# Optimization experiments

Measured on AMD Instinct MI355X. Metric: run time of the kernel, lower is better.

## Reference

```python
import jax, jax.numpy as jnp
import numpy as np

D_MODEL = 1024
N_HEAD = 16
D_HEAD = D_MODEL // N_HEAD


def setup_inputs() -> dict:
    key = jax.random.key(0)
    ks = jax.random.split(key, 5)
    x = jax.random.normal(ks[0], (4, 2048, D_MODEL), dtype=jnp.float32)
    s = 1.0 / np.sqrt(D_MODEL)
    W_qkv = jax.random.normal(ks[1], (D_MODEL, 3 * D_MODEL), dtype=jnp.float32) * s
    b_qkv = jnp.zeros((3 * D_MODEL,), dtype=jnp.float32)
    W_out = jax.random.normal(ks[2], (D_MODEL, D_MODEL), dtype=jnp.float32) * s
    b_out = jnp.zeros((D_MODEL,), dtype=jnp.float32)
    return {"x": x, "W_qkv": W_qkv, "b_qkv": b_qkv, "W_out": W_out, "b_out": b_out}


def reference(x, W_qkv, b_qkv, W_out, b_out):
    B, T, C = x.shape
    qkv = x @ W_qkv + b_qkv                      # [B,T,3C]
    q, k, v = jnp.split(qkv, 3, axis=-1)
    def heads(t):
        return t.reshape(B, T, N_HEAD, D_HEAD).transpose(0, 2, 1, 3)  # [B,H,T,Dh]
    q, k, v = heads(q), heads(k), heads(v)
    scale = 1.0 / np.sqrt(D_HEAD)
    attn = jnp.einsum('bhqd,bhkd->bhqk', q, k) * scale  # [B,H,T,T]
    causal = jnp.tril(jnp.ones((T, T), dtype=bool))
    attn = jnp.where(causal, attn, -jnp.inf)
    attn = jax.nn.softmax(attn, axis=-1)
    out = jnp.einsum('bhqk,bhkd->bhqd', attn, v)  # [B,H,T,Dh]
    out = out.transpose(0, 2, 1, 3).reshape(B, T, C)
    return out @ W_out + b_out
```

## Files before the change

kernel.cpp:

```cpp
#include <hip/hip_runtime.h>

typedef __bf16 bf16;
typedef __bf16 bf16x4 __attribute__((ext_vector_type(4)));
typedef __bf16 bf16x8 __attribute__((ext_vector_type(8)));
typedef float f32x4 __attribute__((ext_vector_type(4)));

#define T_SEQ 2048
#define QK_LD 2048

extern "C" __device__ float __ocml_native_exp2_f32(float);

#define GLOAD16(gp, lp)                                                        \
  __builtin_amdgcn_global_load_lds(                                            \
      (const __attribute__((address_space(1))) unsigned int*)(gp),             \
      (__attribute__((address_space(3))) unsigned int*)(lp), 16, 0, 0)

__global__ void prep_kernel(const float* __restrict__ x, bf16* __restrict__ xb,
                            const float* __restrict__ Wq, bf16* __restrict__ Wtq,
                            const float* __restrict__ Wo, bf16* __restrict__ Wto) {
    __shared__ float tile[32][33];
    const int t = threadIdx.x;
    if (blockIdx.x < 8192) {
        const int i = (blockIdx.x * 256 + t) * 4;
        const float4 f = *(const float4*)(x + i);
        bf16x4 o;
        o.x = (bf16)f.x; o.y = (bf16)f.y; o.z = (bf16)f.z; o.w = (bf16)f.w;
        *(bf16x4*)(xb + i) = o;
        return;
    }
    const int bid = blockIdx.x - 8192;
    const int xblk = bid & 127, yblk = bid >> 7;
    const bool isQ = xblk < 96;
    const float* W = isQ ? Wq : Wo;
    bf16* Wt = isQ ? Wtq : Wto;
    const int C = isQ ? 3072 : 1024;
    const int R = 1024;
    const int bx = (isQ ? xblk : (xblk - 96)) * 32;
    const int by = yblk * 32;
    const int tx = t & 31, ty = t >> 5;
#pragma unroll
    for (int i = 0; i < 32; i += 8)
        tile[ty + i][tx] = W[(size_t)(by + ty + i) * C + bx + tx];
    __syncthreads();
#pragma unroll
    for (int i = 0; i < 32; i += 8)
        Wt[(size_t)(bx + ty + i) * R + by + tx] = (bf16)tile[tx][ty + i];
}

template <bool OUT_BF16, bool SPLIT_V>
__global__ __launch_bounds__(256, 2)
void gemm128(const bf16* __restrict__ A, const bf16* __restrict__ Bt,
             const float* __restrict__ bias, void* __restrict__ Cout,
             bf16* __restrict__ Vtb, int M, int N, int K, int ldC) {
    __shared__ bf16 sm[32768];

    const int t = threadIdx.x;
    const int lane = t & 63, quad = lane >> 4, l16 = lane & 15;
    const int wave = t >> 6;
    const int wm = (wave >> 1) * 64;
    const int wn = (wave & 1) * 64;
    const long m0 = (long)blockIdx.y * 128;
    const long n0 = (long)blockIdx.x * 128;
    (void)M; (void)N;

    f32x4 acc[4][4] = {};

    const int srow = t >> 3;
    const int scol = ((t & 7) ^ ((t >> 3) & 7)) * 8;
    const bf16* agp = A  + (m0 + srow) * (long)K + scol;
    const bf16* bgp = Bt + (n0 + srow) * (long)K + scol;
    const long rowK32 = (long)32 * K;

    auto stage = [&](int buf, int kt) {
        bf16* d = sm + buf * 16384 + t * 8;
        const bf16* a = agp + (long)kt * 64;
        const bf16* b = bgp + (long)kt * 64;
        GLOAD16(a,               d);
        GLOAD16(a +     rowK32,  d + 2048);
        GLOAD16(a + 2 * rowK32,  d + 4096);
        GLOAD16(a + 3 * rowK32,  d + 6144);
        GLOAD16(b,               d + 8192);
        GLOAD16(b +     rowK32,  d + 10240);
        GLOAD16(b + 2 * rowK32,  d + 12288);
        GLOAD16(b + 3 * rowK32,  d + 14336);
    };

    int offA[4][2], offB[4][2];
#pragma unroll
    for (int i = 0; i < 4; ++i)
#pragma unroll
        for (int ks = 0; ks < 2; ++ks) {
            const int rA = wm + i * 16 + l16;
            offA[i][ks] = rA * 64 + (((ks * 4 + quad) ^ (rA & 7)) << 3);
            const int rB = wn + i * 16 + l16;
            offB[i][ks] = 8192 + rB * 64 + (((ks * 4 + quad) ^ (rB & 7)) << 3);
        }

    const int nkt = K >> 6;

    stage(0, 0);
    asm volatile("s_waitcnt vmcnt(0)" ::: "memory");
    __builtin_amdgcn_s_barrier();
    __builtin_amdgcn_sched_barrier(0);

    for (int kt = 0; kt < nkt; ++kt) {
        const int buf = kt & 1;
        if (kt + 1 < nkt) stage(buf ^ 1, kt + 1);
        const bf16* base_ = sm + buf * 16384;
        bf16x8 fA[2][4], fB[2][4];
#pragma unroll
        for (int ks = 0; ks < 2; ++ks)
#pragma unroll
            for (int i = 0; i < 4; ++i) {
                fA[ks][i] = *(const bf16x8*)(base_ + offA[i][ks]);
                fB[ks][i] = *(const bf16x8*)(base_ + offB[i][ks]);
            }
#pragma unroll
        for (int ks = 0; ks < 2; ++ks)
#pragma unroll
            for (int i = 0; i < 4; ++i)
#pragma unroll
                for (int j = 0; j < 4; ++j)
                    acc[i][j] = __builtin_amdgcn_mfma_f32_16x16x32_bf16(
                        fB[ks][j], fA[ks][i], acc[i][j], 0, 0, 0);
        if (kt + 1 < nkt) {
            asm volatile("s_waitcnt vmcnt(0)" ::: "memory");
            __builtin_amdgcn_s_barrier();
            __builtin_amdgcn_sched_barrier(0);
        }
    }

    bf16*  Cb = (bf16*)Cout;
    float* Cf = (float*)Cout;
    const bool vblock = SPLIT_V && (n0 >= 2048);
#pragma unroll
    for (int i = 0; i < 4; ++i) {
        const long gm = m0 + wm + i * 16 + l16;
#pragma unroll
        for (int j = 0; j < 4; ++j) {
            const int nloc = wn + j * 16 + quad * 4;
            const long n = n0 + nloc;
            const float4 bv = *(const float4*)(bias + n);
            float v[4];
#pragma unroll
            for (int r = 0; r < 4; ++r) v[r] = acc[i][j][r] + (&bv.x)[r];
            if (vblock) {
                const int bb = (int)(gm >> 11), tok = (int)(gm & 2047);
                const int nv = (int)(n - 2048);
                const int h = nv >> 6, d0 = nv & 63;
                bf16* dst = Vtb + ((size_t)(bb * 16 + h) * 64 + d0) * T_SEQ + tok;
#pragma unroll
                for (int r = 0; r < 4; ++r) dst[(size_t)r * T_SEQ] = (bf16)v[r];
            } else if (OUT_BF16) {
                bf16x4 o;
#pragma unroll
                for (int r = 0; r < 4; ++r) o[r] = (bf16)v[r];
                *(bf16x4*)(Cb + gm * ldC + n) = o;
            } else {
                float4 o;
#pragma unroll
                for (int r = 0; r < 4; ++r) (&o.x)[r] = v[r];
                *(float4*)(Cf + gm * ldC + n) = o;
            }
        }
    }
}

__global__ __launch_bounds__(256, 3)
void attn_kernel(const bf16* __restrict__ qk, const bf16* __restrict__ vtb,
                 bf16* __restrict__ Out) {
    const int bh = blockIdx.x;
    const int qt = 15 - (int)blockIdx.y;
    const int b = bh >> 4, h = bh & 15;
    const int t = threadIdx.x;
    const int wave = t >> 6, lane = t & 63, quad = lane >> 4, l16 = lane & 15;
    const int wq = wave * 32;
    const int q0 = qt * 128;

    __shared__ bf16 Ks[2][4096];
    __shared__ bf16 VTs[2][4096];
    __shared__ bf16 Ps[8192];

    const bf16* Qg = qk + (size_t)b * T_SEQ * QK_LD + h * 64;
    const bf16* Kg = Qg + 1024;
    const bf16* vth = vtb + (size_t)bh * 64 * T_SEQ;

    for (int c = t; c < 1024; c += 256) {
        const int row = c >> 3, kb = c & 7;
        *(uint4*)(Ps + row * 64 + (((kb ^ (row & 7)) << 3))) =
            *(const uint4*)(Qg + (size_t)(q0 + row) * QK_LD + kb * 8);
    }
    __syncthreads();
    const float qsc = 0.125f * 1.4426950408889634f;
    bf16x8 qf[2][2];
#pragma unroll
    for (int jt = 0; jt < 2; ++jt)
#pragma unroll
        for (int s = 0; s < 2; ++s) {
            const int row = wq + jt * 16 + l16;
            bf16x8 v = *(const bf16x8*)(Ps + row * 64 + (((s * 4 + quad) ^ (row & 7)) << 3));
#pragma unroll
            for (int e = 0; e < 8; ++e) v[e] = (bf16)((float)v[e] * qsc);
            qf[jt][s] = v;
        }

    const int sr = t >> 3;
    const int skb = (t & 7) ^ (sr & 7);
    const bf16* kp0 = Kg + (size_t)sr * QK_LD + skb * 8;
    const bf16* kp1 = kp0 + (size_t)32 * QK_LD;
    const bf16* vp0 = vth + (size_t)sr * T_SEQ + skb * 8;
    const bf16* vp1 = vp0 + (size_t)32 * T_SEQ;

    int offKV[4][2];
#pragma unroll
    for (int it = 0; it < 4; ++it)
#pragma unroll
        for (int s = 0; s < 2; ++s) {
            const int row = it * 16 + l16;
            offKV[it][s] = row * 64 + (((s * 4 + quad) ^ (row & 7)) << 3);
        }

    f32x4 oacc[4][2] = {};
    float lsum[2] = {0.f, 0.f};
    const int nkt = qt * 2 + 2;

    uint4 kr0 = *(const uint4*)kp0, kr1 = *(const uint4*)kp1;
    uint4 vr0 = *(const uint4*)vp0, vr1 = *(const uint4*)vp1;

    for (int kt = 0; kt < nkt; ++kt) {
        const int k0 = kt * 64;
        bf16* kb_ = Ks[kt & 1];
        bf16* vb_ = VTs[kt & 1];
        *(uint4*)(kb_ + t * 8)        = kr0;
        *(uint4*)(kb_ + 2048 + t * 8) = kr1;
        *(uint4*)(vb_ + t * 8)        = vr0;
        *(uint4*)(vb_ + 2048 + t * 8) = vr1;
        __syncthreads();

        if (kt + 1 < nkt) {
            const int kn = k0 + 64;
            kr0 = *(const uint4*)(kp0 + (size_t)kn * QK_LD);
            kr1 = *(const uint4*)(kp1 + (size_t)kn * QK_LD);
            vr0 = *(const uint4*)(vp0 + kn);
            vr1 = *(const uint4*)(vp1 + kn);
        }

        f32x4 sacc[4][2] = {};
#pragma unroll
        for (int s = 0; s < 2; ++s) {
            bf16x8 kf[4];
#pragma unroll
            for (int it = 0; it < 4; ++it)
                kf[it] = *(const bf16x8*)(kb_ + offKV[it][s]);
#pragma unroll
            for (int it = 0; it < 4; ++it)
#pragma unroll
                for (int jt = 0; jt < 2; ++jt)
                    sacc[it][jt] = __builtin_amdgcn_mfma_f32_16x16x32_bf16(kf[it], qf[jt][s], sacc[it][jt], 0, 0, 0);
        }

        const bool need_mask = (kt >= 2 * qt);
#pragma unroll
        for (int it = 0; it < 4; ++it)
#pragma unroll
            for (int jt = 0; jt < 2; ++jt) {
                const int prow = wq + jt * 16 + l16;
                bf16x4 pb;
                if (need_mask) {
                    const int qrow = q0 + prow;
                    const int kbase = k0 + it * 16 + quad * 4;
#pragma unroll
                    for (int r = 0; r < 4; ++r) {
                        const float e = __ocml_native_exp2_f32(sacc[it][jt][r]);
                        const float p = (kbase + r > qrow) ? 0.f : e;
                        lsum[jt] += p;
                        pb[r] = (bf16)p;
                    }
                } else {
#pragma unroll
                    for (int r = 0; r < 4; ++r) {
                        const float p = __ocml_native_exp2_f32(sacc[it][jt][r]);
                        lsum[jt] += p;
                        pb[r] = (bf16)p;
                    }
                }
                *(bf16x4*)(Ps + prow * 64 +
                           (((it * 2 + (quad >> 1)) ^ (prow & 7)) << 3) + ((quad & 1) << 2)) = pb;
            }

#pragma unroll
        for (int s2 = 0; s2 < 2; ++s2) {
            bf16x8 vf[4], pf[2];
#pragma unroll
            for (int it2 = 0; it2 < 4; ++it2)
                vf[it2] = *(const bf16x8*)(vb_ + offKV[it2][s2]);
#pragma unroll
            for (int jt = 0; jt < 2; ++jt) {
                const int prow = wq + jt * 16 + l16;
                pf[jt] = *(const bf16x8*)(Ps + prow * 64 + (((s2 * 4 + quad) ^ (prow & 7)) << 3));
            }
#pragma unroll
            for (int it2 = 0; it2 < 4; ++it2)
#pragma unroll
                for (int jt = 0; jt < 2; ++jt)
                    oacc[it2][jt] = __builtin_amdgcn_mfma_f32_16x16x32_bf16(vf[it2], pf[jt], oacc[it2][jt], 0, 0, 0);
        }
    }

    float inv[2];
#pragma unroll
    for (int jt = 0; jt < 2; ++jt) {
        float l = lsum[jt];
        l += __shfl_xor(l, 16);
        l += __shfl_xor(l, 32);
        inv[jt] = 1.0f / l;
    }
#pragma unroll
    for (int it2 = 0; it2 < 4; ++it2)
#pragma unroll
        for (int jt = 0; jt < 2; ++jt) {
            bf16x4 ob;
#pragma unroll
            for (int r = 0; r < 4; ++r) ob[r] = (bf16)(oacc[it2][jt][r] * inv[jt]);
            const int qrow = q0 + wq + jt * 16 + l16;
            const int dcol = h * 64 + it2 * 16 + quad * 4;
            *(bf16x4*)&Out[(size_t)(b * T_SEQ + qrow) * 1024 + dcol] = ob;
        }
}

extern "C" void kernel_launch(void* const* d_in, const int* in_sizes, int n_in,
                              void* d_out, int out_size, void* d_ws, size_t ws_size,
                              hipStream_t stream) {
    const float* x     = (const float*)d_in[0];
    const float* W_qkv = (const float*)d_in[1];
    const float* b_qkv = (const float*)d_in[2];
    const float* W_out = (const float*)d_in[3];
    const float* b_out = (const float*)d_in[4];
    float* out = (float*)d_out;

    char* ws = (char*)d_ws;
    bf16* xb   = (bf16*)ws; ws += (size_t)8192 * 1024 * 2;
    bf16* wtq  = (bf16*)ws; ws += (size_t)3072 * 1024 * 2;
    bf16* wto  = (bf16*)ws; ws += (size_t)1024 * 1024 * 2;
    bf16* qkb  = (bf16*)ws; ws += (size_t)8192 * 2048 * 2;
    bf16* vtb  = (bf16*)ws; ws += (size_t)64 * 64 * 2048 * 2;
    bf16* aout = (bf16*)ws; ws += (size_t)8192 * 1024 * 2;

    prep_kernel<<<8192 + 4096, 256, 0, stream>>>(x, xb, W_qkv, wtq, W_out, wto);

    gemm128<true, true><<<dim3(24, 64), 256, 0, stream>>>(
        xb, wtq, b_qkv, (void*)qkb, vtb, 8192, 3072, 1024, 2048);
    attn_kernel<<<dim3(64, 16), 256, 0, stream>>>(qkb, vtb, aout);
    gemm128<false, false><<<dim3(8, 64), 256, 0, stream>>>(
        aout, wto, b_out, (void*)out, nullptr, 8192, 1024, 1024, 1024);
}
```

Before: 232.4 us.

## Restructure GEMM mainloop to 4-stage K=32 LDS pipeline with partial vmcnt waits

The GEMM main loop moves from a double-buffered K=64 tile with a full vmcnt(0) wait each iteration to a four-buffer ring of K=32 tiles. Three tiles are kept in flight, and a partial vmcnt wait lets global-to-LDS loads overlap MFMA compute. The LDS swizzle and fragment offsets are reworked for the 32-wide rows. In exchange there are twice as many barriers per K, each compute step has less MFMA work to hide latency, and the swizzle may introduce bank conflicts.

```diff
diff --git a/kernel.cpp b/kernel.cpp
--- a/kernel.cpp
+++ b/kernel.cpp
@@ -65,70 +65,69 @@
 
     f32x4 acc[4][4] = {};
 
-    const int srow = t >> 3;
-    const int scol = ((t & 7) ^ ((t >> 3) & 7)) * 8;
+    const int srow = t >> 2;
+    const int scol = ((t & 3) ^ ((t >> 3) & 3)) * 8;
     const bf16* agp = A  + (m0 + srow) * (long)K + scol;
     const bf16* bgp = Bt + (n0 + srow) * (long)K + scol;
-    const long rowK32 = (long)32 * K;
+    const long rowK64 = (long)64 * K;
 
     auto stage = [&](int buf, int kt) {
-        bf16* d = sm + buf * 16384 + t * 8;
-        const bf16* a = agp + (long)kt * 64;
-        const bf16* b = bgp + (long)kt * 64;
-        GLOAD16(a,               d);
-        GLOAD16(a +     rowK32,  d + 2048);
-        GLOAD16(a + 2 * rowK32,  d + 4096);
-        GLOAD16(a + 3 * rowK32,  d + 6144);
-        GLOAD16(b,               d + 8192);
-        GLOAD16(b +     rowK32,  d + 10240);
-        GLOAD16(b + 2 * rowK32,  d + 12288);
-        GLOAD16(b + 3 * rowK32,  d + 14336);
+        bf16* d = sm + buf * 8192 + t * 8;
+        const bf16* a = agp + (long)kt * 32;
+        const bf16* b = bgp + (long)kt * 32;
+        GLOAD16(a,          d);
+        GLOAD16(a + rowK64, d + 2048);
+        GLOAD16(b,          d + 4096);
+        GLOAD16(b + rowK64, d + 6144);
     };
 
-    int offA[4][2], offB[4][2];
-#pragma unroll
-    for (int i = 0; i < 4; ++i)
-#pragma unroll
-        for (int ks = 0; ks < 2; ++ks) {
-            const int rA = wm + i * 16 + l16;
-            offA[i][ks] = rA * 64 + (((ks * 4 + quad) ^ (rA & 7)) << 3);
-            const int rB = wn + i * 16 + l16;
-            offB[i][ks] = 8192 + rB * 64 + (((ks * 4 + quad) ^ (rB & 7)) << 3);
-        }
-
-    const int nkt = K >> 6;
+    int offA[4], offB[4];
+#pragma unroll
+    for (int i = 0; i < 4; ++i) {
+        const int rA = wm + i * 16 + l16;
+        offA[i] = rA * 32 + ((quad ^ ((rA >> 1) & 3)) * 8);
+        const int rB = wn + i * 16 + l16;
+        offB[i] = 4096 + rB * 32 + ((quad ^ ((rB >> 1) & 3)) * 8);
+    }
+
+    auto compute = [&](int buf) {
+        const bf16* base_ = sm + buf * 8192;
+        bf16x8 fA[4], fB[4];
+#pragma unroll
+        for (int i = 0; i < 4; ++i) {
+            fA[i] = *(const bf16x8*)(base_ + offA[i]);
+            fB[i] = *(const bf16x8*)(base_ + offB[i]);
+        }
+#pragma unroll
+        for (int i = 0; i < 4; ++i)
+#pragma unroll
+            for (int j = 0; j < 4; ++j)
+                acc[i][j] = __builtin_amdgcn_mfma_f32_16x16x32_bf16(
+                    fB[j], fA[i], acc[i][j], 0, 0, 0);
+    };
+
+    const int nkt = K >> 5;
 
     stage(0, 0);
+    stage(1, 1);
+    stage(2, 2);
+
+    for (int kt = 0; kt < nkt - 3; ++kt) {
+        stage((kt + 3) & 3, kt + 3);
+        asm volatile("s_waitcnt vmcnt(12)" ::: "memory");
+        __builtin_amdgcn_s_barrier();
+        compute(kt & 3);
+        __builtin_amdgcn_s_barrier();
+    }
+    asm volatile("s_waitcnt vmcnt(8)" ::: "memory");
+    __builtin_amdgcn_s_barrier();
+    compute((nkt - 3) & 3);
+    asm volatile("s_waitcnt vmcnt(4)" ::: "memory");
+    __builtin_amdgcn_s_barrier();
+    compute((nkt - 2) & 3);
     asm volatile("s_waitcnt vmcnt(0)" ::: "memory");
     __builtin_amdgcn_s_barrier();
-    __builtin_amdgcn_sched_barrier(0);
-
-    for (int kt = 0; kt < nkt; ++kt) {
-        const int buf = kt & 1;
-        if (kt + 1 < nkt) stage(buf ^ 1, kt + 1);
-        const bf16* base_ = sm + buf * 16384;
-        bf16x8 fA[2][4], fB[2][4];
-#pragma unroll
-        for (int ks = 0; ks < 2; ++ks)
-#pragma unroll
-            for (int i = 0; i < 4; ++i) {
-                fA[ks][i] = *(const bf16x8*)(base_ + offA[i][ks]);
-                fB[ks][i] = *(const bf16x8*)(base_ + offB[i][ks]);
-            }
-#pragma unroll
-        for (int ks = 0; ks < 2; ++ks)
-#pragma unroll
-            for (int i = 0; i < 4; ++i)
-#pragma unroll
-                for (int j = 0; j < 4; ++j)
-                    acc[i][j] = __builtin_amdgcn_mfma_f32_16x16x32_bf16(
-                        fB[ks][j], fA[ks][i], acc[i][j], 0, 0, 0);
-        if (kt + 1 < nkt) {
-            asm volatile("s_waitcnt vmcnt(0)" ::: "memory");
-            __builtin_amdgcn_s_barrier();
-            __builtin_amdgcn_sched_barrier(0);
-        }
-    }
+    compute((nkt - 1) & 3);
 
     bf16*  Cb = (bf16*)Cout;
     float* Cf = (float*)Cout;
```

Result: slower. 241.1 us (+3.8%).

## Stage K/V tiles via async global-to-LDS loads and raise MFMA wave priority

Applied to the files above, without the earlier changes.

Replaces the register-staged K/V prefetch with direct global_load_lds copies into the double-buffered shared tiles. The first tile is issued before the Q load, and each next tile is issued at the top of the loop, followed by a vmcnt wait and barrier at the loop end. This removes the register round trip and the LDS store instructions and frees VGPRs. It also wraps the MFMA blocks in s_setprio so matrix work is favoured over other waves. There is a risk that the single end-of-iteration barrier no longer protects the Ps buffer, which is reused between the softmax write and the PV read across waves.

```diff
diff --git a/kernel.cpp b/kernel.cpp
--- a/kernel.cpp
+++ b/kernel.cpp
@@ -185,25 +185,6 @@
     const bf16* Kg = Qg + 1024;
     const bf16* vth = vtb + (size_t)bh * 64 * T_SEQ;
 
-    for (int c = t; c < 1024; c += 256) {
-        const int row = c >> 3, kb = c & 7;
-        *(uint4*)(Ps + row * 64 + (((kb ^ (row & 7)) << 3))) =
-            *(const uint4*)(Qg + (size_t)(q0 + row) * QK_LD + kb * 8);
-    }
-    __syncthreads();
-    const float qsc = 0.125f * 1.4426950408889634f;
-    bf16x8 qf[2][2];
-#pragma unroll
-    for (int jt = 0; jt < 2; ++jt)
-#pragma unroll
-        for (int s = 0; s < 2; ++s) {
-            const int row = wq + jt * 16 + l16;
-            bf16x8 v = *(const bf16x8*)(Ps + row * 64 + (((s * 4 + quad) ^ (row & 7)) << 3));
-#pragma unroll
-            for (int e = 0; e < 8; ++e) v[e] = (bf16)((float)v[e] * qsc);
-            qf[jt][s] = v;
-        }
-
     const int sr = t >> 3;
     const int skb = (t & 7) ^ (sr & 7);
     const bf16* kp0 = Kg + (size_t)sr * QK_LD + skb * 8;
@@ -211,6 +192,34 @@
     const bf16* vp0 = vth + (size_t)sr * T_SEQ + skb * 8;
     const bf16* vp1 = vp0 + (size_t)32 * T_SEQ;
 
+    auto stageKV = [&](int buf, int k0) {
+        GLOAD16(kp0 + (size_t)k0 * QK_LD, &Ks[buf][t * 8]);
+        GLOAD16(kp1 + (size_t)k0 * QK_LD, &Ks[buf][2048 + t * 8]);
+        GLOAD16(vp0 + k0,                 &VTs[buf][t * 8]);
+        GLOAD16(vp1 + k0,                 &VTs[buf][2048 + t * 8]);
+    };
+
+    stageKV(0, 0);
+
+    for (int c = t; c < 1024; c += 256) {
+        const int row = c >> 3, kb = c & 7;
+        *(uint4*)(Ps + row * 64 + (((kb ^ (row & 7)) << 3))) =
+            *(const uint4*)(Qg + (size_t)(q0 + row) * QK_LD + kb * 8);
+    }
+    __syncthreads();
+    const float qsc = 0.125f * 1.4426950408889634f;
+    bf16x8 qf[2][2];
+#pragma unroll
+    for (int jt = 0; jt < 2; ++jt)
+#pragma unroll
+        for (int s = 0; s < 2; ++s) {
+            const int row = wq + jt * 16 + l16;
+            bf16x8 v = *(const bf16x8*)(Ps + row * 64 + (((s * 4 + quad) ^ (row & 7)) << 3));
+#pragma unroll
+            for (int e = 0; e < 8; ++e) v[e] = (bf16)((float)v[e] * qsc);
+            qf[jt][s] = v;
+        }
+
     int offKV[4][2];
 #pragma unroll
     for (int it = 0; it < 4; ++it)
@@ -224,26 +233,11 @@
     float lsum[2] = {0.f, 0.f};
     const int nkt = qt * 2 + 2;
 
-    uint4 kr0 = *(const uint4*)kp0, kr1 = *(const uint4*)kp1;
-    uint4 vr0 = *(const uint4*)vp0, vr1 = *(const uint4*)vp1;
-
     for (int kt = 0; kt < nkt; ++kt) {
         const int k0 = kt * 64;
-        bf16* kb_ = Ks[kt & 1];
-        bf16* vb_ = VTs[kt & 1];
-        *(uint4*)(kb_ + t * 8)        = kr0;
-        *(uint4*)(kb_ + 2048 + t * 8) = kr1;
-        *(uint4*)(vb_ + t * 8)        = vr0;
-        *(uint4*)(vb_ + 2048 + t * 8) = vr1;
-        __syncthreads();
-
-        if (kt + 1 < nkt) {
-            const int kn = k0 + 64;
-            kr0 = *(const uint4*)(kp0 + (size_t)kn * QK_LD);
-            kr1 = *(const uint4*)(kp1 + (size_t)kn * QK_LD);
-            vr0 = *(const uint4*)(vp0 + kn);
-            vr1 = *(const uint4*)(vp1 + kn);
-        }
+        if (kt + 1 < nkt) stageKV((kt + 1) & 1, k0 + 64);
+        const bf16* kb_ = Ks[kt & 1];
+        const bf16* vb_ = VTs[kt & 1];
 
         f32x4 sacc[4][2] = {};
 #pragma unroll
@@ -252,11 +246,13 @@
 #pragma unroll
             for (int it = 0; it < 4; ++it)
                 kf[it] = *(const bf16x8*)(kb_ + offKV[it][s]);
+            __builtin_amdgcn_s_setprio(1);
 #pragma unroll
             for (int it = 0; it < 4; ++it)
 #pragma unroll
                 for (int jt = 0; jt < 2; ++jt)
                     sacc[it][jt] = __builtin_amdgcn_mfma_f32_16x16x32_bf16(kf[it], qf[jt][s], sacc[it][jt], 0, 0, 0);
+            __builtin_amdgcn_s_setprio(0);
         }
 
         const bool need_mask = (kt >= 2 * qt);
@@ -299,11 +295,18 @@
                 const int prow = wq + jt * 16 + l16;
                 pf[jt] = *(const bf16x8*)(Ps + prow * 64 + (((s2 * 4 + quad) ^ (prow & 7)) << 3));
             }
+            __builtin_amdgcn_s_setprio(1);
 #pragma unroll
             for (int it2 = 0; it2 < 4; ++it2)
 #pragma unroll
                 for (int jt = 0; jt < 2; ++jt)
                     oacc[it2][jt] = __builtin_amdgcn_mfma_f32_16x16x32_bf16(vf[it2], pf[jt], oacc[it2][jt], 0, 0, 0);
+            __builtin_amdgcn_s_setprio(0);
+        }
+
+        if (kt + 1 < nkt) {
+            asm volatile("s_waitcnt vmcnt(0)" ::: "memory");
+            __builtin_amdgcn_s_barrier();
         }
     }
 
```

Result: slower. 244.6 us (+5.3%).

## Add BK=32 QKV GEMM variant with higher occupancy; raise MFMA priority in attention

Applied to the files above, without the earlier changes.

Adds a new 128x128 GEMM kernel with a 32-wide K step and half the shared memory, declared for four blocks per CU, and uses it for the QKV projection. Smaller LDS tiles let more blocks stay resident to hide load latency, but each block does twice as many barrier-separated iterations. Attention MFMA sections are also wrapped in s_setprio to favour matrix issue over the softmax/exp work of other waves.

```diff
diff --git a/kernel.cpp b/kernel.cpp
--- a/kernel.cpp
+++ b/kernel.cpp
@@ -45,6 +45,115 @@
 #pragma unroll
     for (int i = 0; i < 32; i += 8)
         Wt[(size_t)(bx + ty + i) * R + by + tx] = (bf16)tile[tx][ty + i];
+}
+
+template <bool OUT_BF16, bool SPLIT_V>
+__global__ __launch_bounds__(256, 4)
+void gemm128_32(const bf16* __restrict__ A, const bf16* __restrict__ Bt,
+                const float* __restrict__ bias, void* __restrict__ Cout,
+                bf16* __restrict__ Vtb, int M, int N, int K, int ldC) {
+    __shared__ bf16 sm[16384];
+
+    const int t = threadIdx.x;
+    const int lane = t & 63, quad = lane >> 4, l16 = lane & 15;
+    const int wave = t >> 6;
+    const int wm = (wave >> 1) * 64;
+    const int wn = (wave & 1) * 64;
+    const long m0 = (long)blockIdx.y * 128;
+    const long n0 = (long)blockIdx.x * 128;
+    (void)M; (void)N;
+
+    f32x4 acc[4][4] = {};
+
+    const int srow = t >> 2;
+    const int scol = ((t & 3) ^ ((t >> 3) & 3)) * 8;
+    const bf16* agp = A  + (m0 + srow) * (long)K + scol;
+    const bf16* bgp = Bt + (n0 + srow) * (long)K + scol;
+    const long rowK64 = (long)64 * K;
+
+    auto stage = [&](int buf, int kt) {
+        bf16* d = sm + buf * 8192 + t * 8;
+        const bf16* a = agp + (long)kt * 32;
+        const bf16* b = bgp + (long)kt * 32;
+        GLOAD16(a,          d);
+        GLOAD16(a + rowK64, d + 2048);
+        GLOAD16(b,          d + 4096);
+        GLOAD16(b + rowK64, d + 6144);
+    };
+
+    int offA[4], offB[4];
+#pragma unroll
+    for (int i = 0; i < 4; ++i) {
+        const int rA = wm + i * 16 + l16;
+        offA[i] = rA * 32 + ((quad ^ ((rA >> 1) & 3)) * 8);
+        const int rB = wn + i * 16 + l16;
+        offB[i] = 4096 + rB * 32 + ((quad ^ ((rB >> 1) & 3)) * 8);
+    }
+
+    const int nkt = K >> 5;
+
+    stage(0, 0);
+    asm volatile("s_waitcnt vmcnt(0)" ::: "memory");
+    __builtin_amdgcn_s_barrier();
+    __builtin_amdgcn_sched_barrier(0);
+
+    for (int kt = 0; kt < nkt; ++kt) {
+        const int buf = kt & 1;
+        if (kt + 1 < nkt) stage(buf ^ 1, kt + 1);
+        const bf16* base_ = sm + buf * 8192;
+        bf16x8 fA[4], fB[4];
+#pragma unroll
+        for (int i = 0; i < 4; ++i) {
+            fA[i] = *(const bf16x8*)(base_ + offA[i]);
+            fB[i] = *(const bf16x8*)(base_ + offB[i]);
+        }
+#pragma unroll
+        for (int i = 0; i < 4; ++i)
+#pragma unroll
+            for (int j = 0; j < 4; ++j)
+                acc[i][j] = __builtin_amdgcn_mfma_f32_16x16x32_bf16(
+                    fB[j], fA[i], acc[i][j], 0, 0, 0);
+        if (kt + 1 < nkt) {
+            asm volatile("s_waitcnt vmcnt(0)" ::: "memory");
+            __builtin_amdgcn_s_barrier();
+            __builtin_amdgcn_sched_barrier(0);
+        }
+    }
+
+    bf16*  Cb = (bf16*)Cout;
+    float* Cf = (float*)Cout;
+    const bool vblock = SPLIT_V && (n0 >= 2048);
+#pragma unroll
+    for (int i = 0; i < 4; ++i) {
+        const long gm = m0 + wm + i * 16 + l16;
+#pragma unroll
+        for (int j = 0; j < 4; ++j) {
+            const int nloc = wn + j * 16 + quad * 4;
+            const long n = n0 + nloc;
+            const float4 bv = *(const float4*)(bias + n);
+            float v[4];
+#pragma unroll
+            for (int r = 0; r < 4; ++r) v[r] = acc[i][j][r] + (&bv.x)[r];
+            if (vblock) {
+                const int bb = (int)(gm >> 11), tok = (int)(gm & 2047);
+                const int nv = (int)(n - 2048);
+                const int h = nv >> 6, d0 = nv & 63;
+                bf16* dst = Vtb + ((size_t)(bb * 16 + h) * 64 + d0) * T_SEQ + tok;
+#pragma unroll
+                for (int r = 0; r < 4; ++r) dst[(size_t)r * T_SEQ] = (bf16)v[r];
+            } else if (OUT_BF16) {
+                bf16x4 o;
+#pragma unroll
+                for (int r = 0; r < 4; ++r) o[r] = (bf16)v[r];
+                *(bf16x4*)(Cb + gm * ldC + n) = o;
+            } else {
+                float4 o;
+#pragma unroll
+                for (int r = 0; r < 4; ++r) (&o.x)[r] = v[r];
+                *(float4*)(Cf + gm * ldC + n) = o;
+            }
+        }
+    }
 }
 
 template <bool OUT_BF16, bool SPLIT_V>
@@ -252,11 +361,13 @@
 #pragma unroll
             for (int it = 0; it < 4; ++it)
                 kf[it] = *(const bf16x8*)(kb_ + offKV[it][s]);
+            __builtin_amdgcn_s_setprio(1);
 #pragma unroll
             for (int it = 0; it < 4; ++it)
 #pragma unroll
                 for (int jt = 0; jt < 2; ++jt)
                     sacc[it][jt] = __builtin_amdgcn_mfma_f32_16x16x32_bf16(kf[it], qf[jt][s], sacc[it][jt], 0, 0, 0);
+            __builtin_amdgcn_s_setprio(0);
         }
 
         const bool need_mask = (kt >= 2 * qt);
@@ -299,11 +410,13 @@
                 const int prow = wq + jt * 16 + l16;
                 pf[jt] = *(const bf16x8*)(Ps + prow * 64 + (((s2 * 4 + quad) ^ (prow & 7)) << 3));
             }
+            __builtin_amdgcn_s_setprio(1);
 #pragma unroll
             for (int it2 = 0; it2 < 4; ++it2)
 #pragma unroll
                 for (int jt = 0; jt < 2; ++jt)
                     oacc[it2][jt] = __builtin_amdgcn_mfma_f32_16x16x32_bf16(vf[it2], pf[jt], oacc[it2][jt], 0, 0, 0);
+            __builtin_amdgcn_s_setprio(0);
         }
     }
 
@@ -348,7 +461,7 @@
 
     prep_kernel<<<8192 + 4096, 256, 0, stream>>>(x, xb, W_qkv, wtq, W_out, wto);
 
-    gemm128<true, true><<<dim3(24, 64), 256, 0, stream>>>(
+    gemm128_32<true, true><<<dim3(24, 64), 256, 0, stream>>>(
         xb, wtq, b_qkv, (void*)qkb, vtb, 8192, 3072, 1024, 2048);
     attn_kernel<<<dim3(64, 16), 256, 0, stream>>>(qkb, vtb, aout);
     gemm128<false, false><<<dim3(8, 64), 256, 0, stream>>>(
```

New measurement: 242.2 us. 1.04x slower.
